# Optimization experiments

Hardware: AMD Instinct MI355X
Metric: run time of the kernel (lower is better)

The kernel has to match this reference:

```python
import jax, jax.numpy as jnp
import numpy as np

NUM_CODEBOOKS = 4
NUM_VECTORS = 1024
DIM = 256
B, T = 16, 4096


def setup_inputs() -> dict:
    key = jax.random.key(0)
    k1, k2 = jax.random.split(key)
    z = jax.random.normal(k1, (B, DIM, T), dtype=jnp.float32)
    # torch init: randn then uniform_(-1/num_vectors, 1/num_vectors) overwrites -> uniform
    codebooks = jax.random.uniform(
        k2, (NUM_CODEBOOKS, NUM_VECTORS, DIM), dtype=jnp.float32,
        minval=-1.0 / NUM_VECTORS, maxval=1.0 / NUM_VECTORS)
    return {"z": z, "codebooks": codebooks}


def reference(z, codebooks):
    # z: [B, C, T] -> work in token-major layout [B, T, C]
    x = jnp.transpose(z, (0, 2, 1))  # [B, T, C]
    sg = jax.lax.stop_gradient

    residual = x
    z_q = jnp.zeros_like(x)
    indices_list = []
    loss_total = jnp.float32(0.0)
    for i in range(codebooks.shape[0]):
        cb = codebooks[i]  # [V, C]
        # squared L2 distances: ||r||^2 + ||c||^2 - 2 r.c
        d = (jnp.sum(residual ** 2, axis=-1, keepdims=True)
             + jnp.sum(cb ** 2, axis=-1)
             - 2.0 * jnp.einsum('btc,vc->btv', residual, cb))  # [B, T, V]
        idx = jnp.argmin(d, axis=-1)        # [B, T]
        q = cb[idx]                          # [B, T, C] gather
        # straight-through estimator
        zq_i = residual + sg(q - residual)
        # commitment: mse(z_q.detach(), residual); z_q here equals q numerically
        loss_total = loss_total + jnp.mean((sg(zq_i) - residual) ** 2)
        z_q = z_q + zq_i
        residual = residual - sg(zq_i)
        indices_list.append(idx)

    loss = loss_total / codebooks.shape[0]
    indices = jnp.stack(indices_list, axis=1)      # [B, K, T]
    z_q_out = jnp.transpose(z_q, (0, 2, 1))        # [B, C, T]
    return z_q_out, indices, loss
```

## Files before the change

### kernel.cpp

```cpp
#include <hip/hip_runtime.h>
#include <math.h>

#define B_   16
#define C_   256
#define T_   4096
#define V_   1024
#define K_   4
#define TPB  64
#define RTP  66
#define EPS_CAND 2e-4f

constexpr int Z_ELEMS   = B_ * C_ * T_;
constexpr int IDX_ELEMS = B_ * K_ * T_;
constexpr int LOSS_OFF  = Z_ELEMS + IDX_ELEMS;

typedef _Float16 h4 __attribute__((ext_vector_type(4)));
typedef float    f4 __attribute__((ext_vector_type(4)));

__global__ void rvq_zero_loss(float* out) { out[LOSS_OFF] = 0.0f; }

__global__ void rvq_cvnorm(const float* __restrict__ cb, float2* __restrict__ cvw)
{
    int g = blockIdx.x * 256 + threadIdx.x;
    const float* row = cb + (size_t)g * C_;
    float p0 = 0.f, p1 = 0.f;
    for (int c = 0;   c < 64;  ++c) p0 = fmaf(row[c], row[c], p0);
    for (int c = 128; c < 192; ++c) p0 = fmaf(row[c], row[c], p0);
    for (int c = 64;  c < 128; ++c) p1 = fmaf(row[c], row[c], p1);
    for (int c = 192; c < 256; ++c) p1 = fmaf(row[c], row[c], p1);
    cvw[g] = make_float2(p0, p1);
}

__global__ void rvq_cbf16(const float* __restrict__ cb, _Float16* __restrict__ cbh)
{
    int gid = blockIdx.x * 256 + threadIdx.x;
    int l  = gid & 63;
    int ks = (gid >> 6) & 15;
    int nt = (gid >> 10) & 63;
    int st = gid >> 16;
    int v  = nt * 16 + (l & 15);
    int k  = ks * 16 + 4 * (l >> 4);
    const float* src = cb + ((size_t)(st * V_ + v)) * C_ + k;
    float4 cv = *reinterpret_cast<const float4*>(src);
    h4 o;
    o[0] = (_Float16)(cv.x * 16.0f);
    o[1] = (_Float16)(cv.y * 16.0f);
    o[2] = (_Float16)(cv.z * 16.0f);
    o[3] = (_Float16)(cv.w * 16.0f);
    reinterpret_cast<h4*>(cbh)[gid] = o;
}

__launch_bounds__(512, 4)
__global__ void rvq_main(const float* __restrict__ z,
                         const float* __restrict__ cb,
                         const float2* __restrict__ cvw,
                         const _Float16* __restrict__ cbh,
                         float* __restrict__ out)
{
    __shared__ float Rt[C_][RTP];
    __shared__ float gmin[8][TPB];
    __shared__ float fmin[TPB];
    __shared__ int   candCnt[TPB];
    __shared__ int   candIdx[TPB][16];
    __shared__ float pbD[TPB][16];
    __shared__ int   bestIdx[TPB];
    __shared__ float rnpart[TPB][8];
    __shared__ float Rnorm[TPB];

    const int tid = threadIdx.x;
    const int blk = blockIdx.x;
    const int b   = blk >> 6;
    const int t0  = (blk & 63) * TPB;

    const int w   = tid >> 6;
    const int l   = tid & 63;
    const int ut  = tid & 63;
    const int ug  = tid >> 6;

    const float* zb = z + (size_t)b * C_ * T_ + t0;
    for (int j = 0; j < 32; ++j) {
        int c = ug * 32 + j;
        Rt[c][ut] = zb[(size_t)c * T_ + ut];
    }
    __syncthreads();
    {
        float p = 0.f;
        for (int j = 0; j < 32; ++j) { float r = Rt[ug * 32 + j][ut]; p = fmaf(r, r, p); }
        rnpart[ut][ug] = p;
    }
    __syncthreads();
    if (tid < TPB) {
        float s = rnpart[tid][0];
        for (int k = 1; k < 8; ++k) s = __fadd_rn(s, rnpart[tid][k]);
        Rnorm[tid] = s;
    }
    __syncthreads();

    float loss_acc = 0.f;

    const int am   = l & 15;
    const int akof = (l >> 4) * 4;

    for (int st = 0; st < K_; ++st) {
        const float* cbs = cb + (size_t)st * V_ * C_;

        for (int p = 0; p < 2; ++p) {
            const int vbase = p * 512 + w * 64;

            f4 acc[4][4];
            #pragma unroll
            for (int mt = 0; mt < 4; ++mt)
                #pragma unroll
                for (int nf = 0; nf < 4; ++nf)
                    acc[mt][nf] = (f4){0.f, 0.f, 0.f, 0.f};

            {
                const h4* cbh4 = reinterpret_cast<const h4*>(cbh);
                const size_t wbase = (size_t)st * 65536 + (size_t)(vbase >> 4) * 1024 + l;
                #pragma unroll 4
                for (int ks = 0; ks < 16; ++ks) {
                    const int kk = ks * 16 + akof;
                    h4 af[4];
                    #pragma unroll
                    for (int mt = 0; mt < 4; ++mt) {
                        const int m = mt * 16 + am;
                        h4 a;
                        a[0] = (_Float16)Rt[kk + 0][m];
                        a[1] = (_Float16)Rt[kk + 1][m];
                        a[2] = (_Float16)Rt[kk + 2][m];
                        a[3] = (_Float16)Rt[kk + 3][m];
                        af[mt] = a;
                    }
                    #pragma unroll
                    for (int nf = 0; nf < 4; ++nf) {
                        h4 bf = cbh4[wbase + (size_t)nf * 1024 + ks * 64];
                        #pragma unroll
                        for (int mt = 0; mt < 4; ++mt)
                            acc[mt][nf] = __builtin_amdgcn_mfma_f32_16x16x16f16(af[mt], bf, acc[mt][nf], 0, 0, 0);
                    }
                }
            }

            float cv2v[4];
            #pragma unroll
            for (int nf = 0; nf < 4; ++nf) {
                int v = vbase + nf * 16 + (l & 15);
                float2 pv = cvw[st * V_ + v];
                cv2v[nf] = __fadd_rn(pv.x, pv.y);
            }
            #pragma unroll
            for (int mt = 0; mt < 4; ++mt)
                #pragma unroll
                for (int nf = 0; nf < 4; ++nf)
                    #pragma unroll
                    for (int jj = 0; jj < 4; ++jj)
                        acc[mt][nf][jj] = fmaf(acc[mt][nf][jj], -0.125f, cv2v[nf]);

            float tmin[4][4];
            #pragma unroll
            for (int mt = 0; mt < 4; ++mt)
                #pragma unroll
                for (int jj = 0; jj < 4; ++jj) {
                    float m0 = acc[mt][0][jj];
                    #pragma unroll
                    for (int nf = 1; nf < 4; ++nf) m0 = fminf(m0, acc[mt][nf][jj]);
                    tmin[mt][jj] = m0;
                }
            #pragma unroll
            for (int mt = 0; mt < 4; ++mt)
                #pragma unroll
                for (int jj = 0; jj < 4; ++jj) {
                    float m0 = tmin[mt][jj];
                    m0 = fminf(m0, __shfl_xor(m0, 1, 16));
                    m0 = fminf(m0, __shfl_xor(m0, 2, 16));
                    m0 = fminf(m0, __shfl_xor(m0, 4, 16));
                    m0 = fminf(m0, __shfl_xor(m0, 8, 16));
                    tmin[mt][jj] = m0;
                }
            if ((l & 15) == 0) {
                #pragma unroll
                for (int mt = 0; mt < 4; ++mt)
                    #pragma unroll
                    for (int jj = 0; jj < 4; ++jj)
                        gmin[w][mt * 16 + 4 * (l >> 4) + jj] = tmin[mt][jj];
            }
            __syncthreads();
            if (tid < TPB) {
                float mm = gmin[0][tid];
                #pragma unroll
                for (int ww = 1; ww < 8; ++ww) mm = fminf(mm, gmin[ww][tid]);
                fmin[tid] = mm;
                if (p == 0) candCnt[tid] = 0;
            }
            __syncthreads();

            {
                float fthr[4][4];
                #pragma unroll
                for (int mt = 0; mt < 4; ++mt)
                    #pragma unroll
                    for (int jj = 0; jj < 4; ++jj)
                        fthr[mt][jj] = fmin[mt * 16 + 4 * (l >> 4) + jj] + EPS_CAND;
                #pragma unroll
                for (int mt = 0; mt < 4; ++mt)
                    #pragma unroll
                    for (int nf = 0; nf < 4; ++nf)
                        #pragma unroll
                        for (int jj = 0; jj < 4; ++jj)
                            if (acc[mt][nf][jj] <= fthr[mt][jj]) {
                                int tok = mt * 16 + 4 * (l >> 4) + jj;
                                int s = atomicAdd(&candCnt[tok], 1);
                                if (s < 16) candIdx[tok][s] = vbase + nf * 16 + (l & 15);
                            }
            }
            __syncthreads();
        }

        {
            int t = tid & 63, s0 = tid >> 6;
            int nc = candCnt[t]; if (nc > 16) nc = 16;
            for (int s = s0; s < nc; s += 8) {
                int gi = candIdx[t][s];
                const float* crow = cbs + (size_t)gi * C_;
                float dot = 0.f;
                for (int c = 0; c < 256; c += 4) {
                    float4 cr = *reinterpret_cast<const float4*>(crow + c);
                    dot = __fadd_rn(dot, __fmul_rn(Rt[c + 0][t], cr.x));
                    dot = __fadd_rn(dot, __fmul_rn(Rt[c + 1][t], cr.y));
                    dot = __fadd_rn(dot, __fmul_rn(Rt[c + 2][t], cr.z));
                    dot = __fadd_rn(dot, __fmul_rn(Rt[c + 3][t], cr.w));
                }
                float2 pv = cvw[st * V_ + gi];
                float cv2 = __fadd_rn(pv.x, pv.y);
                float S = __fadd_rn(Rnorm[t], cv2);
                pbD[t][s] = __fsub_rn(S, 2.0f * dot);
            }
        }
        __syncthreads();
        if (tid < TPB) {
            int nc = candCnt[tid]; if (nc > 16) nc = 16;
            float bd = pbD[tid][0];
            int   bi = candIdx[tid][0];
            for (int s = 1; s < nc; ++s) {
                float d  = pbD[tid][s];
                int   i2 = candIdx[tid][s];
                if (d < bd || (d == bd && i2 < bi)) { bd = d; bi = i2; }
            }
            bestIdx[tid] = bi;
            out[Z_ELEMS + ((size_t)b * K_ + st) * T_ + t0 + tid] = (float)bi;
        }
        __syncthreads();

        {
            const float* q = cbs + (size_t)bestIdx[ut] * C_ + ug * 32;
            float rn = 0.f;
            for (int j4 = 0; j4 < 8; ++j4) {
                float4 qv = *reinterpret_cast<const float4*>(q + 4 * j4);
                float qe[4] = { qv.x, qv.y, qv.z, qv.w };
                #pragma unroll
                for (int e = 0; e < 4; ++e) {
                    int c = ug * 32 + 4 * j4 + e;
                    float r   = Rt[c][ut];
                    float qmr = __fsub_rn(qe[e], r);
                    float zq  = __fadd_rn(r, qmr);
                    float lt  = __fsub_rn(zq, r);
                    loss_acc  = fmaf(lt, lt, loss_acc);
                    float rn2 = __fsub_rn(r, zq);
                    Rt[c][ut] = rn2;
                    rn = fmaf(rn2, rn2, rn);
                }
            }
            rnpart[ut][ug] = rn;
        }
        __syncthreads();
        if (tid < TPB) {
            float s = rnpart[tid][0];
            for (int k = 1; k < 8; ++k) s = __fadd_rn(s, rnpart[tid][k]);
            Rnorm[tid] = s;
        }
        __syncthreads();
    }

    {
        float* ob = out + (size_t)b * C_ * T_ + t0;
        for (int j = 0; j < 32; ++j) {
            int c = ug * 32 + j;
            ob[(size_t)c * T_ + ut] = __fsub_rn(zb[(size_t)c * T_ + ut], Rt[c][ut]);
        }
    }

    __syncthreads();
    float* lred = &gmin[0][0];
    lred[tid] = loss_acc;
    __syncthreads();
    if (tid < 256) lred[tid] += lred[tid + 256];
    __syncthreads();
    if (tid < 128) lred[tid] += lred[tid + 128];
    __syncthreads();
    if (tid < 64)  lred[tid] += lred[tid + 64];
    __syncthreads();
    if (tid == 0) {
        float s = 0.f;
        for (int i = 0; i < 64; ++i) s += lred[i];
        atomicAdd(out + LOSS_OFF, s * (1.0f / 67108864.0f));
    }
}

extern "C" void kernel_launch(void* const* d_in, const int* in_sizes, int n_in,
                              void* d_out, int out_size, void* d_ws, size_t ws_size,
                              hipStream_t stream)
{
    const float* z  = (const float*)d_in[0];
    const float* cb = (const float*)d_in[1];
    float* out = (float*)d_out;
    float2*    cvw = (float2*)d_ws;
    _Float16*  cbh = (_Float16*)((char*)d_ws + 32768);

    rvq_zero_loss<<<1, 1, 0, stream>>>(out);
    rvq_cvnorm<<<16, 256, 0, stream>>>(cb, cvw);
    rvq_cbf16<<<1024, 256, 0, stream>>>(cb, cbh);
    rvq_main<<<dim3(1024), dim3(512), 0, stream>>>(z, cb, cvw, cbh, out);
}
```

Baseline: 492.9 us.

## Switch distance GEMM to 16x16x32 MFMA with 32x128 per-wave tiles

Repacks the fp16 codebook into 8-element K fragments and switches the distance GEMM to the 16x16x32 f16 MFMA instruction. Each wave now covers 32 tokens by 128 codes instead of 64 tokens by 64 codes, which halves the number of MFMA issues and changes how A and B fragments are reused. The separate block-wide min reduction and one barrier are removed: each wave computes its threshold directly from the four gmin rows for its token half. The cost is more B loads per wave and fewer A reuses, and it relies on the 16x16x32 MFMA being available on this GPU.

```diff
diff --git a/kernel.cpp b/kernel.cpp
--- a/kernel.cpp
+++ b/kernel.cpp
@@ -14,7 +14,7 @@
 constexpr int IDX_ELEMS = B_ * K_ * T_;
 constexpr int LOSS_OFF  = Z_ELEMS + IDX_ELEMS;
 
-typedef _Float16 h4 __attribute__((ext_vector_type(4)));
+typedef _Float16 h8 __attribute__((ext_vector_type(8)));
 typedef float    f4 __attribute__((ext_vector_type(4)));
 
 __global__ void rvq_zero_loss(float* out) { out[LOSS_OFF] = 0.0f; }
@@ -35,19 +35,24 @@
 {
     int gid = blockIdx.x * 256 + threadIdx.x;
     int l  = gid & 63;
-    int ks = (gid >> 6) & 15;
-    int nt = (gid >> 10) & 63;
-    int st = gid >> 16;
+    int ks = (gid >> 6) & 7;
+    int nt = (gid >> 9) & 63;
+    int st = gid >> 15;
     int v  = nt * 16 + (l & 15);
-    int k  = ks * 16 + 4 * (l >> 4);
+    int k  = ks * 32 + (l >> 4) * 8;
     const float* src = cb + ((size_t)(st * V_ + v)) * C_ + k;
-    float4 cv = *reinterpret_cast<const float4*>(src);
-    h4 o;
-    o[0] = (_Float16)(cv.x * 16.0f);
-    o[1] = (_Float16)(cv.y * 16.0f);
-    o[2] = (_Float16)(cv.z * 16.0f);
-    o[3] = (_Float16)(cv.w * 16.0f);
-    reinterpret_cast<h4*>(cbh)[gid] = o;
+    float4 c0 = *reinterpret_cast<const float4*>(src);
+    float4 c1 = *reinterpret_cast<const float4*>(src + 4);
+    h8 o;
+    o[0] = (_Float16)(c0.x * 16.0f);
+    o[1] = (_Float16)(c0.y * 16.0f);
+    o[2] = (_Float16)(c0.z * 16.0f);
+    o[3] = (_Float16)(c0.w * 16.0f);
+    o[4] = (_Float16)(c1.x * 16.0f);
+    o[5] = (_Float16)(c1.y * 16.0f);
+    o[6] = (_Float16)(c1.z * 16.0f);
+    o[7] = (_Float16)(c1.w * 16.0f);
+    reinterpret_cast<h8*>(cbh)[gid] = o;
 }
 
 __launch_bounds__(512, 4)
@@ -59,7 +64,6 @@
 {
     __shared__ float Rt[C_][RTP];
     __shared__ float gmin[8][TPB];
-    __shared__ float fmin[TPB];
     __shared__ int   candCnt[TPB];
     __shared__ int   candIdx[TPB][16];
     __shared__ float pbD[TPB][16];
@@ -74,6 +78,8 @@
 
     const int w   = tid >> 6;
     const int l   = tid & 63;
+    const int wv  = w >> 1;
+    const int th  = (w & 1) * 32;
     const int ut  = tid & 63;
     const int ug  = tid >> 6;
 
@@ -99,119 +105,103 @@
     float loss_acc = 0.f;
 
     const int am   = l & 15;
-    const int akof = (l >> 4) * 4;
+    const int akof = (l >> 4) * 8;
 
     for (int st = 0; st < K_; ++st) {
         const float* cbs = cb + (size_t)st * V_ * C_;
 
         for (int p = 0; p < 2; ++p) {
-            const int vbase = p * 512 + w * 64;
-
-            f4 acc[4][4];
+            const int vbase = p * 512 + wv * 128;
+
+            f4 acc[2][8];
             #pragma unroll
-            for (int mt = 0; mt < 4; ++mt)
-                #pragma unroll
-                for (int nf = 0; nf < 4; ++nf)
+            for (int mt = 0; mt < 2; ++mt)
+                #pragma unroll
+                for (int nf = 0; nf < 8; ++nf)
                     acc[mt][nf] = (f4){0.f, 0.f, 0.f, 0.f};
 
             {
-                const h4* cbh4 = reinterpret_cast<const h4*>(cbh);
-                const size_t wbase = (size_t)st * 65536 + (size_t)(vbase >> 4) * 1024 + l;
-                #pragma unroll 4
-                for (int ks = 0; ks < 16; ++ks) {
-                    const int kk = ks * 16 + akof;
-                    h4 af[4];
-                    #pragma unroll
-                    for (int mt = 0; mt < 4; ++mt) {
-                        const int m = mt * 16 + am;
-                        h4 a;
-                        a[0] = (_Float16)Rt[kk + 0][m];
-                        a[1] = (_Float16)Rt[kk + 1][m];
-                        a[2] = (_Float16)Rt[kk + 2][m];
-                        a[3] = (_Float16)Rt[kk + 3][m];
+                const h8* cbh8 = reinterpret_cast<const h8*>(cbh);
+                const size_t wbase = ((size_t)(st * 64 + (vbase >> 4)) * 8) * 64 + l;
+                #pragma unroll 2
+                for (int ks = 0; ks < 8; ++ks) {
+                    const int k0 = ks * 32 + akof;
+                    h8 af[2];
+                    #pragma unroll
+                    for (int mt = 0; mt < 2; ++mt) {
+                        const int m = th + mt * 16 + am;
+                        h8 a;
+                        #pragma unroll
+                        for (int i = 0; i < 8; ++i)
+                            a[i] = (_Float16)Rt[k0 + i][m];
                         af[mt] = a;
                     }
                     #pragma unroll
-                    for (int nf = 0; nf < 4; ++nf) {
-                        h4 bf = cbh4[wbase + (size_t)nf * 1024 + ks * 64];
+                    for (int nf = 0; nf < 8; ++nf) {
+                        h8 bf = cbh8[wbase + (size_t)(nf * 8 + ks) * 64];
                         #pragma unroll
-                        for (int mt = 0; mt < 4; ++mt)
-                            acc[mt][nf] = __builtin_amdgcn_mfma_f32_16x16x16f16(af[mt], bf, acc[mt][nf], 0, 0, 0);
+                        for (int mt = 0; mt < 2; ++mt)
+                            acc[mt][nf] = __builtin_amdgcn_mfma_f32_16x16x32_f16(af[mt], bf, acc[mt][nf], 0, 0, 0);
                     }
                 }
             }
 
-            float cv2v[4];
+            float cv2v[8];
             #pragma unroll
-            for (int nf = 0; nf < 4; ++nf) {
-                int v = vbase + nf * 16 + (l & 15);
+            for (int nf = 0; nf < 8; ++nf) {
+                int v = vbase + nf * 16 + am;
                 float2 pv = cvw[st * V_ + v];
                 cv2v[nf] = __fadd_rn(pv.x, pv.y);
             }
             #pragma unroll
-            for (int mt = 0; mt < 4; ++mt)
-                #pragma unroll
-                for (int nf = 0; nf < 4; ++nf)
+            for (int mt = 0; mt < 2; ++mt)
+                #pragma unroll
+                for (int nf = 0; nf < 8; ++nf)
                     #pragma unroll
                     for (int jj = 0; jj < 4; ++jj)
                         acc[mt][nf][jj] = fmaf(acc[mt][nf][jj], -0.125f, cv2v[nf]);
 
-            float tmin[4][4];
+            float tmin[2][4];
             #pragma unroll
-            for (int mt = 0; mt < 4; ++mt)
+            for (int mt = 0; mt < 2; ++mt)
                 #pragma unroll
                 for (int jj = 0; jj < 4; ++jj) {
                     float m0 = acc[mt][0][jj];
                     #pragma unroll
-                    for (int nf = 1; nf < 4; ++nf) m0 = fminf(m0, acc[mt][nf][jj]);
-                    tmin[mt][jj] = m0;
-                }
-            #pragma unroll
-            for (int mt = 0; mt < 4; ++mt)
-                #pragma unroll
-                for (int jj = 0; jj < 4; ++jj) {
-                    float m0 = tmin[mt][jj];
+                    for (int nf = 1; nf < 8; ++nf) m0 = fminf(m0, acc[mt][nf][jj]);
                     m0 = fminf(m0, __shfl_xor(m0, 1, 16));
                     m0 = fminf(m0, __shfl_xor(m0, 2, 16));
                     m0 = fminf(m0, __shfl_xor(m0, 4, 16));
                     m0 = fminf(m0, __shfl_xor(m0, 8, 16));
                     tmin[mt][jj] = m0;
                 }
-            if ((l & 15) == 0) {
-                #pragma unroll
-                for (int mt = 0; mt < 4; ++mt)
+            if (am == 0) {
+                #pragma unroll
+                for (int mt = 0; mt < 2; ++mt)
                     #pragma unroll
                     for (int jj = 0; jj < 4; ++jj)
-                        gmin[w][mt * 16 + 4 * (l >> 4) + jj] = tmin[mt][jj];
-            }
+                        gmin[w][th + mt * 16 + 4 * (l >> 4) + jj] = tmin[mt][jj];
+            }
+            if (p == 0 && tid < TPB) candCnt[tid] = 0;
             __syncthreads();
-            if (tid < TPB) {
-                float mm = gmin[0][tid];
-                #pragma unroll
-                for (int ww = 1; ww < 8; ++ww) mm = fminf(mm, gmin[ww][tid]);
-                fmin[tid] = mm;
-                if (p == 0) candCnt[tid] = 0;
-            }
-            __syncthreads();
 
             {
-                float fthr[4][4];
-                #pragma unroll
-                for (int mt = 0; mt < 4; ++mt)
-                    #pragma unroll
-                    for (int jj = 0; jj < 4; ++jj)
-                        fthr[mt][jj] = fmin[mt * 16 + 4 * (l >> 4) + jj] + EPS_CAND;
-                #pragma unroll
-                for (int mt = 0; mt < 4; ++mt)
-                    #pragma unroll
-                    for (int nf = 0; nf < 4; ++nf)
+                const int wb = w & 1;
+                #pragma unroll
+                for (int mt = 0; mt < 2; ++mt)
+                    #pragma unroll
+                    for (int jj = 0; jj < 4; ++jj) {
+                        int t = th + mt * 16 + 4 * (l >> 4) + jj;
+                        float fm = fminf(fminf(gmin[wb][t], gmin[wb + 2][t]),
+                                         fminf(gmin[wb + 4][t], gmin[wb + 6][t]));
+                        float fthr = fm + EPS_CAND;
                         #pragma unroll
-                        for (int jj = 0; jj < 4; ++jj)
-                            if (acc[mt][nf][jj] <= fthr[mt][jj]) {
-                                int tok = mt * 16 + 4 * (l >> 4) + jj;
-                                int s = atomicAdd(&candCnt[tok], 1);
-                                if (s < 16) candIdx[tok][s] = vbase + nf * 16 + (l & 15);
+                        for (int nf = 0; nf < 8; ++nf)
+                            if (acc[mt][nf][jj] <= fthr) {
+                                int s = atomicAdd(&candCnt[t], 1);
+                                if (s < 16) candIdx[t][s] = vbase + nf * 16 + am;
                             }
+                    }
             }
             __syncthreads();
         }
@@ -318,6 +308,6 @@
 
     rvq_zero_loss<<<1, 1, 0, stream>>>(out);
     rvq_cvnorm<<<16, 256, 0, stream>>>(cb, cvw);
-    rvq_cbf16<<<1024, 256, 0, stream>>>(cb, cbh);
+    rvq_cbf16<<<512, 256, 0, stream>>>(cb, cbh);
     rvq_main<<<dim3(1024), dim3(512), 0, stream>>>(z, cb, cvw, cbh, out);
 }
```

After: 489.2 us. About the same (-0.8%).
